# Kernel tuning notes

Measured on AMD Instinct MI355X. Metric: run time of the kernel, lower is better.

Reference implementation:

```python
import jax, jax.numpy as jnp
import numpy as np

N_NODES = 100000
N_EDGES = 1600000
F_IN = 64
HID = 64
N_CLASSES = 45
N_GRAPHS = 256


def gcn_conv(x, src, dst, W, b, n):
    # GCNConv with added self-loops and symmetric normalization (PyG semantics)
    h = x @ W  # [N, H]
    deg = jax.ops.segment_sum(jnp.ones(src.shape[0], h.dtype), dst, num_segments=n) + 1.0
    dinv = jax.lax.rsqrt(deg)  # deg^{-1/2}, deg >= 1 due to self loops
    coef = dinv[src] * dinv[dst]  # [E]
    msg = h[src] * coef[:, None]  # gather + scale
    agg = jax.ops.segment_sum(msg, dst, num_segments=n)  # scatter-add to dst
    agg = agg + h * (dinv * dinv)[:, None]  # self-loop contribution
    return agg + b


def setup_inputs() -> dict:
    key = jax.random.key(0)
    ks = jax.random.split(key, 12)
    x = jax.random.normal(ks[0], (N_NODES, F_IN), dtype=jnp.float32)
    edge_index = jax.random.randint(ks[1], (2, N_EDGES), 0, N_NODES, dtype=jnp.int32)
    batch = jnp.sort(jax.random.randint(ks[2], (N_NODES,), 0, N_GRAPHS, dtype=jnp.int32))
    s1 = 1.0 / np.sqrt(F_IN)
    s2 = 1.0 / np.sqrt(HID)
    W1 = jax.random.uniform(ks[3], (F_IN, HID), jnp.float32, -s1, s1)
    b1 = jnp.zeros((HID,), jnp.float32)
    W2 = jax.random.uniform(ks[4], (HID, HID), jnp.float32, -s2, s2)
    b2 = jnp.zeros((HID,), jnp.float32)
    W3 = jax.random.uniform(ks[5], (HID, HID), jnp.float32, -s2, s2)
    b3 = jnp.zeros((HID,), jnp.float32)
    Wl = jax.random.uniform(ks[6], (HID, N_CLASSES), jnp.float32, -s2, s2)
    bl = jnp.zeros((N_CLASSES,), jnp.float32)
    return {"x": x, "edge_index": edge_index, "batch": batch,
            "W1": W1, "b1": b1, "W2": W2, "b2": b2, "W3": W3, "b3": b3,
            "Wl": Wl, "bl": bl}


def reference(x, edge_index, batch, W1, b1, W2, b2, W3, b3, Wl, bl):
    n = x.shape[0]
    src, dst = edge_index[0], edge_index[1]
    h = jax.nn.relu(gcn_conv(x, src, dst, W1, b1, n))
    h = jax.nn.relu(gcn_conv(h, src, dst, W2, b2, n))
    h = gcn_conv(h, src, dst, W3, b3, n)
    # global mean pool over graph segments
    sums = jax.ops.segment_sum(h, batch, num_segments=N_GRAPHS)  # [G, H]
    cnts = jax.ops.segment_sum(jnp.ones(n, h.dtype), batch, num_segments=N_GRAPHS)
    pooled = sums / jnp.maximum(cnts, 1.0)[:, None]
    # dropout is identity in eval mode
    return pooled @ Wl + bl  # [G, num_classes]
```

## Files before the change

### kernel.cpp

```cpp
#include <hip/hip_runtime.h>
#include <hip/hip_bf16.h>

#define N_NODES   100000
#define N_EDGES   1600000
#define F_IN      64
#define HID       64
#define N_CLASSES 45
#define N_GRAPHS  256
#define SB        392
#define NPB       256
#define CAP       4608
#define WPB       72
#define CHUNK     4096
#define NCHUNK    391
#define NZB       192
#define GEMM_GRID 782
#define AGGE_GRID 7056
#define NZB2      192
#define ZLEN4_F   1600000
#define ZLEN4_A   1604096
#define LW        72

typedef __attribute__((ext_vector_type(8))) short bf16x8;
typedef __attribute__((ext_vector_type(4))) float f32x4;
union B128 { uint4 u; bf16x8 b; };

__device__ __forceinline__ float rl_f(float v, int k) {
    return __uint_as_float(__builtin_amdgcn_readlane(__float_as_uint(v), k));
}
__device__ __forceinline__ int rl_i(int v, int k) {
    return __builtin_amdgcn_readlane(v, k);
}
__device__ __forceinline__ unsigned short f2bf(float x) {
    unsigned u = __float_as_uint(x);
    unsigned r = u + 0x7FFFu + ((u >> 16) & 1u);
    return (unsigned short)(r >> 16);
}
__device__ __forceinline__ float bf2f(unsigned short h) {
    return __uint_as_float(((unsigned)h) << 16);
}
__device__ __forceinline__ unsigned scale2(unsigned u, float dv) {
    float lo = __uint_as_float(u << 16) * dv;
    float hi = __uint_as_float(u & 0xFFFF0000u) * dv;
    return (((unsigned)f2bf(hi)) << 16) | (unsigned)f2bf(lo);
}

__global__ __launch_bounds__(256) void k_prep(const float* __restrict__ W1, const float* __restrict__ W2,
                                              const float* __restrict__ W3, unsigned short* __restrict__ Wt) {
    const float* W = (blockIdx.x == 0) ? W1 : (blockIdx.x == 1) ? W2 : W3;
    unsigned short* o = Wt + blockIdx.x * 4096;
    int t = threadIdx.x;
    #pragma unroll
    for (int i = 0; i < 16; i++) {
        int e = i * 256 + t;
        o[e] = f2bf(W[(e & 63) * 64 + (e >> 6)]);
    }
}

__global__ __launch_bounds__(256) void k_front(const int* __restrict__ src, const int* __restrict__ dst,
                                               int* __restrict__ bcur, int* __restrict__ binned,
                                               const float* __restrict__ x, const unsigned short* __restrict__ Wt1,
                                               unsigned short* __restrict__ P, float* __restrict__ zbase) {
    int bid = blockIdx.x;
    int t   = threadIdx.x;
    if (bid < NCHUNK) {
        __shared__ int stg[CHUNK];
        __shared__ unsigned short bkt[CHUNK];
        __shared__ int h[512], cur[512], off[512];
        __shared__ int ps[256];
        h[t] = 0; h[t + 256] = 0;
        __syncthreads();
        int base4 = bid * (CHUNK / 4);
        #pragma unroll
        for (int i = 0; i < CHUNK / 1024; i++) {
            int e4 = base4 + i * 256 + t;
            if (e4 < N_EDGES / 4) {
                int4 d = ((const int4*)dst)[e4];
                atomicAdd(&h[d.x >> 8], 1);
                atomicAdd(&h[d.y >> 8], 1);
                atomicAdd(&h[d.z >> 8], 1);
                atomicAdd(&h[d.w >> 8], 1);
            }
        }
        __syncthreads();
        int a0 = h[2 * t], a1 = h[2 * t + 1];
        ps[t] = a0 + a1;
        __syncthreads();
        for (int o = 1; o < 256; o <<= 1) {
            int v = (t >= o) ? ps[t - o] : 0;
            __syncthreads();
            if (t >= o) ps[t] += v;
            __syncthreads();
        }
        int pex = ps[t] - (a0 + a1);
        int e0 = pex, e1 = pex + a0;
        cur[2 * t] = e0; cur[2 * t + 1] = e1;
        if (2 * t < SB && a0 > 0)
            off[2 * t] = (2 * t) * CAP + atomicAdd(&bcur[2 * t], a0) - e0;
        if (2 * t + 1 < SB && a1 > 0)
            off[2 * t + 1] = (2 * t + 1) * CAP + atomicAdd(&bcur[2 * t + 1], a1) - e1;
        __syncthreads();
        int total = ps[255];
        #pragma unroll
        for (int i = 0; i < CHUNK / 1024; i++) {
            int e4 = base4 + i * 256 + t;
            if (e4 < N_EDGES / 4) {
                int4 d  = ((const int4*)dst)[e4];
                int4 s4 = ((const int4*)src)[e4];
                int q;
                q = atomicAdd(&cur[d.x >> 8], 1); stg[q] = s4.x | ((d.x & 255) << 17); bkt[q] = (unsigned short)(d.x >> 8);
                q = atomicAdd(&cur[d.y >> 8], 1); stg[q] = s4.y | ((d.y & 255) << 17); bkt[q] = (unsigned short)(d.y >> 8);
                q = atomicAdd(&cur[d.z >> 8], 1); stg[q] = s4.z | ((d.z & 255) << 17); bkt[q] = (unsigned short)(d.z >> 8);
                q = atomicAdd(&cur[d.w >> 8], 1); stg[q] = s4.w | ((d.w & 255) << 17); bkt[q] = (unsigned short)(d.w >> 8);
            }
        }
        __syncthreads();
        for (int i = t; i < total; i += 256) {
            int b = bkt[i];
            binned[off[b] + i] = stg[i];
        }
    } else if (bid < NCHUNK + NZB) {
        float4 z = make_float4(0.f, 0.f, 0.f, 0.f);
        float4* zp = (float4*)zbase;
        int zb = bid - NCHUNK;
        for (long i = (long)zb * 256 + t; i < (long)ZLEN4_F; i += (long)NZB * 256)
            zp[i] = z;
    } else {
        __shared__ unsigned short xin_s[128 * LW];
        __shared__ unsigned short wt_s[64 * LW];
        int nb = (bid - NCHUNK - NZB) * 128;
        #pragma unroll
        for (int i = 0; i < 16; i++) {
            int e = i * 256 + t;
            wt_s[(e >> 6) * LW + (e & 63)] = Wt1[e];
        }
        #pragma unroll
        for (int i = 0; i < 8; i++) {
            int f = i * 256 + t;
            int row = f >> 4, q = f & 15;
            int gR = nb + row;
            unsigned u0 = 0, u1 = 0;
            if (gR < N_NODES) {
                float4 xv = ((const float4*)x)[(size_t)gR * 16 + q];
                u0 = ((unsigned)f2bf(xv.y) << 16) | f2bf(xv.x);
                u1 = ((unsigned)f2bf(xv.w) << 16) | f2bf(xv.z);
            }
            *(uint2*)&xin_s[row * LW + q * 4] = make_uint2(u0, u1);
        }
        __syncthreads();
        int lane = t & 63, w = t >> 6;
        int l15 = lane & 15, l4 = lane >> 4;
        B128 bfr[4][2];
        #pragma unroll
        for (int nt = 0; nt < 4; nt++)
            #pragma unroll
            for (int ks = 0; ks < 2; ks++)
                bfr[nt][ks].u = *(const uint4*)&wt_s[(nt * 16 + l15) * LW + ks * 32 + l4 * 8];
        f32x4 acc[2][4] = {};
        #pragma unroll
        for (int m = 0; m < 2; m++) {
            int rb = w * 32 + m * 16;
            B128 a0, a1;
            a0.u = *(const uint4*)&xin_s[(rb + l15) * LW +  0 + l4 * 8];
            a1.u = *(const uint4*)&xin_s[(rb + l15) * LW + 32 + l4 * 8];
            #pragma unroll
            for (int nt = 0; nt < 4; nt++) {
                acc[m][nt] = __builtin_amdgcn_mfma_f32_16x16x32_bf16(a0.b, bfr[nt][0].b, acc[m][nt], 0, 0, 0);
                acc[m][nt] = __builtin_amdgcn_mfma_f32_16x16x32_bf16(a1.b, bfr[nt][1].b, acc[m][nt], 0, 0, 0);
            }
        }
        #pragma unroll
        for (int m = 0; m < 2; m++) {
            int Rbase = nb + w * 32 + m * 16;
            #pragma unroll
            for (int nt = 0; nt < 4; nt++)
                #pragma unroll
                for (int r = 0; r < 4; r++) {
                    int row = Rbase + l4 * 4 + r;
                    if (row < N_NODES)
                        P[(size_t)row * 64 + nt * 16 + l15] = f2bf(acc[m][nt][r]);
                }
        }
    }
}

__global__ __launch_bounds__(1024) void k_bcsr(const int* __restrict__ binned, const int* __restrict__ bcur,
                                               float* __restrict__ dinv, float* __restrict__ dinv2,
                                               int* __restrict__ csr, unsigned short* __restrict__ P) {
    __shared__ int bin_s[CAP];
    __shared__ int cs_s[CAP];
    __shared__ int h[NPB];
    __shared__ int ts[NPB];
    __shared__ float sdv[NPB];
    int t = threadIdx.x;
    int b = blockIdx.x;
    int nb0  = b << 8;
    int ebeg = b * CAP;
    int ecnt = bcur[b]; if (ecnt > CAP) ecnt = CAP;
    if (t < NPB) h[t] = 0;
    __syncthreads();
    for (int i = t; i < ecnt; i += 1024) {
        int p = binned[ebeg + i];
        bin_s[i] = p;
        atomicAdd(&h[p >> 17], 1);
    }
    __syncthreads();
    int c = 0;
    if (t < NPB) { c = h[t]; ts[t] = c; }
    __syncthreads();
    for (int o = 1; o < NPB; o <<= 1) {
        int v = (t >= o && t < NPB) ? ts[t - o] : 0;
        __syncthreads();
        if (t >= o && t < NPB) ts[t] += v;
        __syncthreads();
    }
    if (t < NPB) {
        int n = nb0 + t;
        float dval = 0.f;
        if (n < N_NODES) {
            float inv = 1.0f / (float)(c + 1);
            dinv2[n] = inv;
            dval     = sqrtf(inv);
            dinv[n]  = dval;
        }
        sdv[t] = dval;
        h[t] = ts[t] - c;
    }
    __syncthreads();
    for (int i = t; i < ecnt; i += 1024) {
        int p = bin_s[i];
        int q = atomicAdd(&h[p >> 17], 1);
        cs_s[q] = p;
    }
    __syncthreads();
    for (int i = t; i < ecnt; i += 1024)
        csr[ebeg + i] = cs_s[i];
    for (int i = t; i < NPB * 8; i += 1024) {
        int row = i >> 3;
        int nn  = nb0 + row;
        if (nn >= N_NODES) break;
        float dv = sdv[row];
        uint4* pp = (uint4*)P + (size_t)nn * 8 + (i & 7);
        uint4 v = *pp;
        v.x = scale2(v.x, dv); v.y = scale2(v.y, dv);
        v.z = scale2(v.z, dv); v.w = scale2(v.w, dv);
        *pp = v;
    }
}

template<bool POOLI>
__global__ __launch_bounds__(256) void k_gemm(const float* __restrict__ E,
                                              unsigned short* P,
                                              const unsigned short* __restrict__ Wt,
                                              const float* __restrict__ bprev,
                                              const float* __restrict__ bcurr,
                                              const float* __restrict__ dinv,
                                              const float* __restrict__ dinv2,
                                              const int* __restrict__ batch,
                                              float* __restrict__ pool) {
    __shared__ unsigned short xin_s[128 * LW];
    __shared__ unsigned short wt_s[64 * LW];
    int t  = threadIdx.x;
    int nb = blockIdx.x * 128;
    #pragma unroll
    for (int i = 0; i < 16; i++) {
        int e = i * 256 + t;
        wt_s[(e >> 6) * LW + (e & 63)] = Wt[e];
    }
    #pragma unroll
    for (int i = 0; i < 8; i++) {
        int f = i * 256 + t;
        int row = f >> 4, q = f & 15;
        int gR = nb + row;
        unsigned u0 = 0, u1 = 0;
        if (gR < N_NODES) {
            float4  ev = ((const float4*)E)[(size_t)gR * 16 + q];
            ushort4 pv = ((const ushort4*)P)[(size_t)gR * 16 + q];
            float dn = dinv[gR];
            float4 bp = ((const float4*)bprev)[q];
            float x0 = fmaxf(ev.x + fmaf(bf2f(pv.x), dn, bp.x), 0.f);
            float x1 = fmaxf(ev.y + fmaf(bf2f(pv.y), dn, bp.y), 0.f);
            float x2 = fmaxf(ev.z + fmaf(bf2f(pv.z), dn, bp.z), 0.f);
            float x3 = fmaxf(ev.w + fmaf(bf2f(pv.w), dn, bp.w), 0.f);
            u0 = ((unsigned)f2bf(x1) << 16) | f2bf(x0);
            u1 = ((unsigned)f2bf(x3) << 16) | f2bf(x2);
        }
        *(uint2*)&xin_s[row * LW + q * 4] = make_uint2(u0, u1);
    }
    __syncthreads();
    int lane = t & 63, w = t >> 6;
    int l15 = lane & 15, l4 = lane >> 4;
    B128 bfr[4][2];
    #pragma unroll
    for (int nt = 0; nt < 4; nt++)
        #pragma unroll
        for (int ks = 0; ks < 2; ks++)
            bfr[nt][ks].u = *(const uint4*)&wt_s[(nt * 16 + l15) * LW + ks * 32 + l4 * 8];
    f32x4 acc[2][4] = {};
    #pragma unroll
    for (int m = 0; m < 2; m++) {
        int rb = w * 32 + m * 16;
        B128 a0, a1;
        a0.u = *(const uint4*)&xin_s[(rb + l15) * LW +  0 + l4 * 8];
        a1.u = *(const uint4*)&xin_s[(rb + l15) * LW + 32 + l4 * 8];
        #pragma unroll
        for (int nt = 0; nt < 4; nt++) {
            acc[m][nt] = __builtin_amdgcn_mfma_f32_16x16x32_bf16(a0.b, bfr[nt][0].b, acc[m][nt], 0, 0, 0);
            acc[m][nt] = __builtin_amdgcn_mfma_f32_16x16x32_bf16(a1.b, bfr[nt][1].b, acc[m][nt], 0, 0, 0);
        }
    }
    #pragma unroll
    for (int m = 0; m < 2; m++) {
        int Rbase = nb + w * 32 + m * 16;
        float dnr[4], d2r[4];
        #pragma unroll
        for (int r = 0; r < 4; r++) {
            int row = Rbase + l4 * 4 + r;
            bool v = row < N_NODES;
            dnr[r] = v ? dinv[row] : 0.f;
            d2r[r] = (POOLI && v) ? dinv2[row] : 0.f;
        }
        #pragma unroll
        for (int nt = 0; nt < 4; nt++)
            #pragma unroll
            for (int r = 0; r < 4; r++) {
                int row = Rbase + l4 * 4 + r;
                if (row < N_NODES)
                    P[(size_t)row * 64 + nt * 16 + l15] = f2bf(acc[m][nt][r] * dnr[r]);
            }
        if (POOLI) {
            bool full = (Rbase + 15) < N_NODES;
            int g0 = -1, g15 = -2;
            if (full) { g0 = batch[Rbase]; g15 = batch[Rbase + 15]; }
            if (full && g0 == g15) {
                #pragma unroll
                for (int nt = 0; nt < 4; nt++) {
                    float v = 0.f;
                    #pragma unroll
                    for (int r = 0; r < 4; r++) v = fmaf(acc[m][nt][r], d2r[r], v);
                    v += __shfl_xor(v, 16);
                    v += __shfl_xor(v, 32);
                    if (lane < 16)
                        atomicAdd(&pool[g0 * 64 + nt * 16 + lane], fmaf(16.f, bcurr[nt * 16 + lane], v));
                }
            } else if (Rbase < N_NODES) {
                #pragma unroll
                for (int nt = 0; nt < 4; nt++) {
                    float bc = bcurr[nt * 16 + l15];
                    #pragma unroll
                    for (int r = 0; r < 4; r++) {
                        int row = Rbase + l4 * 4 + r;
                        if (row < N_NODES)
                            atomicAdd(&pool[batch[row] * 64 + nt * 16 + l15], fmaf(acc[m][nt][r], d2r[r], bc));
                    }
                }
            }
        }
    }
}

template<bool POOLEP, bool ZROLE>
__global__ __launch_bounds__(256, 8) void k_agge(const unsigned short* __restrict__ Hbuf,
                                                 const int* __restrict__ csr,
                                                 const int* __restrict__ bcur,
                                                 const float* __restrict__ dinv,
                                                 const int* __restrict__ batch,
                                                 float* __restrict__ Out,
                                                 float* __restrict__ zbase) {
    int t = threadIdx.x;
    if (ZROLE && blockIdx.x >= AGGE_GRID) {
        float4 z = make_float4(0.f, 0.f, 0.f, 0.f);
        float4* zp = (float4*)zbase;
        int zb = blockIdx.x - AGGE_GRID;
        for (long i = (long)zb * 256 + t; i < (long)ZLEN4_A; i += (long)NZB2 * 256)
            zp[i] = z;
        return;
    }
    int wv   = t >> 6;
    int lane = t & 63;
    int wid  = blockIdx.x * 4 + wv;
    int b    = wid / WPB;
    int lw   = wid - b * WPB;
    int used = bcur[b]; if (used > CAP) used = CAP;
    int e0   = lw * 64;
    int rem  = used - e0;
    if (rem <= 0) return;
    if (rem > 64) rem = 64;
    int base = b * CAP + e0;

    int p = 0;
    if (lane < rem) p = csr[base + lane];
    int sv = p & 0x1FFFF;
    int dv = p >> 17;

    int dvp = __shfl_up(dv, 1);
    unsigned long long m0 = __ballot(dv != dvp);
    unsigned mlo = __builtin_amdgcn_readfirstlane((unsigned)m0);
    unsigned mhi = __builtin_amdgcn_readfirstlane((unsigned)(m0 >> 32));
    unsigned long long mask = ((((unsigned long long)mhi) << 32) | mlo) & ~1ull;

    bool contL = (lw > 0);
    bool contR = (e0 + rem < used);

    auto flush1 = [&](int dl, float a, bool atom) {
        int dst = (b << 8) + dl;
        if (dst < N_NODES) {
            float val = dinv[dst] * a;
            if (POOLEP) {
                int g = batch[dst];
                atomicAdd(&Out[g * 64 + lane], val);
            } else if (atom) {
                atomicAdd(&Out[(size_t)dst * 64 + lane], val);
            } else {
                Out[(size_t)dst * 64 + lane] = val;
            }
        }
    };

    int cur = rl_i(dv, 0);
    float acc = 0.f;
    bool first = true;
    int j = 0;
    for (; j + 16 <= rem; j += 16) {
        unsigned short u[16];
        #pragma unroll
        for (int i = 0; i < 16; i++) {
            int s = rl_i(sv, j + i);
            u[i] = Hbuf[(size_t)s * 64 + lane];
        }
        #pragma unroll
        for (int i = 0; i < 16; i++) {
            if ((mask >> (j + i)) & 1) {
                flush1(cur, acc, first && contL); first = false;
                acc = 0.f; cur = rl_i(dv, j + i);
            }
            acc += bf2f(u[i]);
        }
    }
    for (; j < rem; j++) {
        int s0 = rl_i(sv, j);
        unsigned short u0 = Hbuf[(size_t)s0 * 64 + lane];
        if ((mask >> j) & 1) {
            flush1(cur, acc, first && contL); first = false;
            acc = 0.f; cur = rl_i(dv, j);
        }
        acc += bf2f(u0);
    }
    flush1(cur, acc, (first && contL) || contR);
}

__device__ __forceinline__ int lbound(const int* __restrict__ a, int n, int v) {
    int lo = 0, hi = n;
    while (lo < hi) { int m = (lo + hi) >> 1; if (a[m] < v) lo = m + 1; else hi = m; }
    return lo;
}

__global__ __launch_bounds__(64) void k_cls(const float* __restrict__ pool, const int* __restrict__ batch,
                                            const float* __restrict__ Wl, const float* __restrict__ bl,
                                            float* __restrict__ out) {
    __shared__ float pm[64];
    __shared__ int bounds[2];
    int g = blockIdx.x;
    int t = threadIdx.x;
    if (t < 2) bounds[t] = lbound(batch, N_NODES, g + t);
    __syncthreads();
    float cnt = (float)(bounds[1] - bounds[0]);
    pm[t] = pool[g * 64 + t] / fmaxf(cnt, 1.0f);
    __syncthreads();
    if (t < N_CLASSES) {
        float o = bl[t];
        #pragma unroll
        for (int k = 0; k < HID; k++) o = fmaf(pm[k], Wl[k * N_CLASSES + t], o);
        out[g * N_CLASSES + t] = o;
    }
}


extern "C" void kernel_launch(void* const* d_in, const int* in_sizes, int n_in,
                              void* d_out, int out_size, void* d_ws, size_t ws_size,
                              hipStream_t stream) {
    const float* x     = (const float*)d_in[0];
    const int*   eidx  = (const int*)  d_in[1];
    const int*   batch = (const int*)  d_in[2];
    const float* W1 = (const float*)d_in[3];
    const float* b1 = (const float*)d_in[4];
    const float* W2 = (const float*)d_in[5];
    const float* b2 = (const float*)d_in[6];
    const float* W3 = (const float*)d_in[7];
    const float* b3 = (const float*)d_in[8];
    const float* Wl = (const float*)d_in[9];
    const float* bl = (const float*)d_in[10];
    const int* src = eidx;
    const int* dst = eidx + N_EDGES;

    char* p = (char*)d_ws;
    auto alloc = [&](size_t bytes) -> void* {
        void* r = (void*)p;
        p += (bytes + 255) & ~(size_t)255;
        return r;
    };
    float* dinv  = (float*)alloc((size_t)N_NODES * 4);
    float* dinv2 = (float*)alloc((size_t)N_NODES * 4);
    int*   csr   = (int*)  alloc((size_t)SB * CAP * 4);
    unsigned short* P = (unsigned short*)alloc((size_t)N_NODES * 64 * 2);
    float* E1    = (float*)alloc((size_t)N_NODES * 64 * 4);
    float* pool  = (float*)alloc((size_t)N_GRAPHS * 64 * 4);
    float* E2    = (float*)alloc((size_t)N_NODES * 64 * 4);
    int*   bcur  = (int*)  alloc((size_t)SB * 4);
    int*   binned = (int*) alloc((size_t)SB * CAP * 4);
    unsigned short* Wt = (unsigned short*)alloc((size_t)3 * 4096 * 2);

    const int front_grid = NCHUNK + NZB + GEMM_GRID;

    hipMemsetAsync(bcur, 0, (size_t)SB * 4, stream);
    k_prep<<<3, 256, 0, stream>>>(W1, W2, W3, Wt);
    k_front<<<front_grid, 256, 0, stream>>>(src, dst, bcur, binned, x, Wt, P, E1);
    k_bcsr <<<SB, 1024, 0, stream>>>(binned, bcur, dinv, dinv2, csr, P);

    k_agge<false, true ><<<AGGE_GRID + NZB2, 256, 0, stream>>>(P, csr, bcur, dinv, batch, E1, pool);
    k_gemm<false><<<GEMM_GRID, 256, 0, stream>>>(E1, P, Wt + 4096, b1, nullptr, dinv, dinv2, batch, nullptr);
    k_agge<false, false><<<AGGE_GRID, 256, 0, stream>>>(P, csr, bcur, dinv, batch, E2, nullptr);
    k_gemm<true ><<<GEMM_GRID, 256, 0, stream>>>(E2, P, Wt + 8192, b2, b3, dinv, dinv2, batch, pool);
    k_agge<true , false><<<AGGE_GRID, 256, 0, stream>>>(P, csr, bcur, dinv, batch, pool, nullptr);

    k_cls<<<N_GRAPHS, 64, 0, stream>>>(pool, batch, Wl, bl, (float*)d_out);
}
```

Before: 309.2 us.

## Zero only boundary-split rows of aggregation buffers and fold weight prep into other kernels

Removes the bulk zero-fill of the E1/E2 aggregation buffers. Instead, k_bcsr records the nodes that have no edges or whose edge list spans a 64-edge wave boundary, and zeroes only those rows. The separate k_prep launch is dropped: W1 is converted to bf16 inline in the GEMM blocks, and W2/W3 are converted by two extra k_bcsr blocks. The pool buffer is now cleared with a memset. This cuts many megabytes of zero writes and one launch, but it depends on the aggregation kernel writing rows it fully owns without atomics, and every GEMM block now repeats the W1 conversion.

```diff
diff --git a/kernel.cpp b/kernel.cpp
--- a/kernel.cpp
+++ b/kernel.cpp
@@ -13,12 +13,8 @@
 #define WPB       72
 #define CHUNK     4096
 #define NCHUNK    391
-#define NZB       192
 #define GEMM_GRID 782
 #define AGGE_GRID 7056
-#define NZB2      192
-#define ZLEN4_F   1600000
-#define ZLEN4_A   1604096
 #define LW        72
 
 typedef __attribute__((ext_vector_type(8))) short bf16x8;
@@ -45,22 +41,10 @@
     return (((unsigned)f2bf(hi)) << 16) | (unsigned)f2bf(lo);
 }
 
-__global__ __launch_bounds__(256) void k_prep(const float* __restrict__ W1, const float* __restrict__ W2,
-                                              const float* __restrict__ W3, unsigned short* __restrict__ Wt) {
-    const float* W = (blockIdx.x == 0) ? W1 : (blockIdx.x == 1) ? W2 : W3;
-    unsigned short* o = Wt + blockIdx.x * 4096;
-    int t = threadIdx.x;
-    #pragma unroll
-    for (int i = 0; i < 16; i++) {
-        int e = i * 256 + t;
-        o[e] = f2bf(W[(e & 63) * 64 + (e >> 6)]);
-    }
-}
-
 __global__ __launch_bounds__(256) void k_front(const int* __restrict__ src, const int* __restrict__ dst,
                                                int* __restrict__ bcur, int* __restrict__ binned,
-                                               const float* __restrict__ x, const unsigned short* __restrict__ Wt1,
-                                               unsigned short* __restrict__ P, float* __restrict__ zbase) {
+                                               const float* __restrict__ x, const float* __restrict__ W1,
+                                               unsigned short* __restrict__ P) {
     int bid = blockIdx.x;
     int t   = threadIdx.x;
     if (bid < NCHUNK) {
@@ -119,20 +103,14 @@
             int b = bkt[i];
             binned[off[b] + i] = stg[i];
         }
-    } else if (bid < NCHUNK + NZB) {
-        float4 z = make_float4(0.f, 0.f, 0.f, 0.f);
-        float4* zp = (float4*)zbase;
-        int zb = bid - NCHUNK;
-        for (long i = (long)zb * 256 + t; i < (long)ZLEN4_F; i += (long)NZB * 256)
-            zp[i] = z;
     } else {
         __shared__ unsigned short xin_s[128 * LW];
         __shared__ unsigned short wt_s[64 * LW];
-        int nb = (bid - NCHUNK - NZB) * 128;
+        int nb = (bid - NCHUNK) * 128;
         #pragma unroll
         for (int i = 0; i < 16; i++) {
             int e = i * 256 + t;
-            wt_s[(e >> 6) * LW + (e & 63)] = Wt1[e];
+            wt_s[(e >> 6) * LW + (e & 63)] = f2bf(W1[(e & 63) * 64 + (e >> 6)]);
         }
         #pragma unroll
         for (int i = 0; i < 8; i++) {
@@ -186,18 +164,31 @@
 
 __global__ __launch_bounds__(1024) void k_bcsr(const int* __restrict__ binned, const int* __restrict__ bcur,
                                                float* __restrict__ dinv, float* __restrict__ dinv2,
-                                               int* __restrict__ csr, unsigned short* __restrict__ P) {
+                                               int* __restrict__ csr, unsigned short* __restrict__ P,
+                                               const float* __restrict__ W2, const float* __restrict__ W3,
+                                               unsigned short* __restrict__ Wt,
+                                               float* __restrict__ E1, float* __restrict__ E2) {
+    int t = threadIdx.x;
+    int b = blockIdx.x;
+    if (b >= SB) {
+        const float* W = (b == SB) ? W2 : W3;
+        unsigned short* o = Wt + (b - SB) * 4096;
+        for (int i = t; i < 4096; i += 1024)
+            o[i] = f2bf(W[(i & 63) * 64 + (i >> 6)]);
+        return;
+    }
     __shared__ int bin_s[CAP];
     __shared__ int cs_s[CAP];
     __shared__ int h[NPB];
     __shared__ int ts[NPB];
     __shared__ float sdv[NPB];
-    int t = threadIdx.x;
-    int b = blockIdx.x;
+    __shared__ unsigned short zlist[NPB];
+    __shared__ int zcnt;
     int nb0  = b << 8;
     int ebeg = b * CAP;
     int ecnt = bcur[b]; if (ecnt > CAP) ecnt = CAP;
     if (t < NPB) h[t] = 0;
+    if (t == 0) zcnt = 0;
     __syncthreads();
     for (int i = t; i < ecnt; i += 1024) {
         int p = binned[ebeg + i];
@@ -215,16 +206,21 @@
         __syncthreads();
     }
     if (t < NPB) {
-        int n = nb0 + t;
+        int n  = nb0 + t;
+        int el = ts[t] - c;
         float dval = 0.f;
         if (n < N_NODES) {
             float inv = 1.0f / (float)(c + 1);
             dinv2[n] = inv;
             dval     = sqrtf(inv);
             dinv[n]  = dval;
+            if (c == 0 || (el >> 6) != ((el + c - 1) >> 6)) {
+                int q = atomicAdd(&zcnt, 1);
+                zlist[q] = (unsigned short)t;
+            }
         }
         sdv[t] = dval;
-        h[t] = ts[t] - c;
+        h[t] = el;
     }
     __syncthreads();
     for (int i = t; i < ecnt; i += 1024) {
@@ -232,9 +228,16 @@
         int q = atomicAdd(&h[p >> 17], 1);
         cs_s[q] = p;
     }
+    int nz = zcnt;
     __syncthreads();
     for (int i = t; i < ecnt; i += 1024)
         csr[ebeg + i] = cs_s[i];
+    float4 z4 = make_float4(0.f, 0.f, 0.f, 0.f);
+    for (int i = t; i < nz * 16; i += 1024) {
+        size_t row = (size_t)(nb0 + zlist[i >> 4]);
+        ((float4*)E1)[row * 16 + (i & 15)] = z4;
+        ((float4*)E2)[row * 16 + (i & 15)] = z4;
+    }
     for (int i = t; i < NPB * 8; i += 1024) {
         int row = i >> 3;
         int nn  = nb0 + row;
@@ -359,23 +362,14 @@
     }
 }
 
-template<bool POOLEP, bool ZROLE>
+template<bool POOLEP>
 __global__ __launch_bounds__(256, 8) void k_agge(const unsigned short* __restrict__ Hbuf,
                                                  const int* __restrict__ csr,
                                                  const int* __restrict__ bcur,
                                                  const float* __restrict__ dinv,
                                                  const int* __restrict__ batch,
-                                                 float* __restrict__ Out,
-                                                 float* __restrict__ zbase) {
+                                                 float* __restrict__ Out) {
     int t = threadIdx.x;
-    if (ZROLE && blockIdx.x >= AGGE_GRID) {
-        float4 z = make_float4(0.f, 0.f, 0.f, 0.f);
-        float4* zp = (float4*)zbase;
-        int zb = blockIdx.x - AGGE_GRID;
-        for (long i = (long)zb * 256 + t; i < (long)ZLEN4_A; i += (long)NZB2 * 256)
-            zp[i] = z;
-        return;
-    }
     int wv   = t >> 6;
     int lane = t & 63;
     int wid  = blockIdx.x * 4 + wv;
@@ -480,8 +474,8 @@
                               void* d_out, int out_size, void* d_ws, size_t ws_size,
                               hipStream_t stream) {
     const float* x     = (const float*)d_in[0];
-    const int*   eidx  = (const int*)  d_in[1];
-    const int*   batch = (const int*)  d_in[2];
+    const int*   eidx  = (const int*)d_in[1];
+    const int*   batch = (const int*)d_in[2];
     const float* W1 = (const float*)d_in[3];
     const float* b1 = (const float*)d_in[4];
     const float* W2 = (const float*)d_in[5];
@@ -508,20 +502,18 @@
     float* E2    = (float*)alloc((size_t)N_NODES * 64 * 4);
     int*   bcur  = (int*)  alloc((size_t)SB * 4);
     int*   binned = (int*) alloc((size_t)SB * CAP * 4);
-    unsigned short* Wt = (unsigned short*)alloc((size_t)3 * 4096 * 2);
-
-    const int front_grid = NCHUNK + NZB + GEMM_GRID;
+    unsigned short* Wt = (unsigned short*)alloc((size_t)2 * 4096 * 2);
 
     hipMemsetAsync(bcur, 0, (size_t)SB * 4, stream);
-    k_prep<<<3, 256, 0, stream>>>(W1, W2, W3, Wt);
-    k_front<<<front_grid, 256, 0, stream>>>(src, dst, bcur, binned, x, Wt, P, E1);
-    k_bcsr <<<SB, 1024, 0, stream>>>(binned, bcur, dinv, dinv2, csr, P);
-
-    k_agge<false, true ><<<AGGE_GRID + NZB2, 256, 0, stream>>>(P, csr, bcur, dinv, batch, E1, pool);
-    k_gemm<false><<<GEMM_GRID, 256, 0, stream>>>(E1, P, Wt + 4096, b1, nullptr, dinv, dinv2, batch, nullptr);
-    k_agge<false, false><<<AGGE_GRID, 256, 0, stream>>>(P, csr, bcur, dinv, batch, E2, nullptr);
-    k_gemm<true ><<<GEMM_GRID, 256, 0, stream>>>(E2, P, Wt + 8192, b2, b3, dinv, dinv2, batch, pool);
-    k_agge<true , false><<<AGGE_GRID, 256, 0, stream>>>(P, csr, bcur, dinv, batch, pool, nullptr);
+    hipMemsetAsync(pool, 0, (size_t)N_GRAPHS * 64 * 4, stream);
+    k_front<<<NCHUNK + GEMM_GRID, 256, 0, stream>>>(src, dst, bcur, binned, x, W1, P);
+    k_bcsr <<<SB + 2, 1024, 0, stream>>>(binned, bcur, dinv, dinv2, csr, P, W2, W3, Wt, E1, E2);
+
+    k_agge<false><<<AGGE_GRID, 256, 0, stream>>>(P, csr, bcur, dinv, batch, E1);
+    k_gemm<false><<<GEMM_GRID, 256, 0, stream>>>(E1, P, Wt, b1, nullptr, dinv, dinv2, batch, nullptr);
+    k_agge<false><<<AGGE_GRID, 256, 0, stream>>>(P, csr, bcur, dinv, batch, E2);
+    k_gemm<true ><<<GEMM_GRID, 256, 0, stream>>>(E2, P, Wt + 4096, b2, b3, dinv, dinv2, batch, pool);
+    k_agge<true ><<<AGGE_GRID, 256, 0, stream>>>(P, csr, bcur, dinv, batch, pool);
 
     k_cls<<<N_GRAPHS, 64, 0, stream>>>(pool, batch, Wl, bl, (float*)d_out);
 }
```

Result: no change. 308.9 us (-0.1%).
